# Kernel tuning notes

Measured on AMD Instinct MI355X. Metric: run time of the kernel, lower is better.

## Reference

```python
import jax, jax.numpy as jnp
import numpy as np

N = 8192
D = 512

def _row_normalize(m):
    # row-normalize; rows summing to 0 get inverse 0 (inf -> 0 in original)
    rs = m.sum(axis=1, keepdims=True)
    inv = jnp.where(rs == 0, 0.0, 1.0 / rs)
    return m * inv

def setup_inputs() -> dict:
    key = jax.random.key(0)
    k1, k2 = jax.random.split(key)
    qf = jax.random.normal(k1, (N, D), dtype=jnp.float32)
    gf = jax.random.normal(k2, (N, D), dtype=jnp.float32)
    return {"qf": qf, "gf": gf}

def reference(qf, gf):
    # feature = row-normalized squared difference  [N, D]
    feature = _row_normalize((qf - gf) ** 2)
    # adj[i, j] = ||feature_i - feature_j||^2, via GEMM expansion
    sq = jnp.sum(feature * feature, axis=-1)                  # [N]
    adj = sq[:, None] + sq[None, :] - 2.0 * (feature @ feature.T)  # [N, N]
    # symmetrize: elementwise max(adj, adj.T) (equivalent to the masked mix)
    adj = jnp.maximum(adj, adj.T)
    # add identity and row-normalize
    adj = adj + jnp.eye(N, dtype=adj.dtype)
    adj = _row_normalize(adj)
    return adj, feature
```

## Files before the change

### kernel.cpp

```cpp
#include <hip/hip_runtime.h>
#include <hip/hip_bf16.h>

#define N 8192
#define D 512

typedef __attribute__((ext_vector_type(8))) short short8;
typedef __attribute__((ext_vector_type(4))) float f32x4;

__device__ __forceinline__ float block_reduce_256(float v, float* red) {
    #pragma unroll
    for (int o = 1; o < 64; o <<= 1) v += __shfl_xor(v, o, 64);
    int w = threadIdx.x >> 6;
    if ((threadIdx.x & 63) == 0) red[w] = v;
    __syncthreads();
    float tot = red[0] + red[1] + red[2] + red[3];
    __syncthreads();
    return tot;
}

__global__ void feature_kernel(const float* __restrict__ qf, const float* __restrict__ gf,
                               float* __restrict__ feat, __hip_bfloat16* __restrict__ featb,
                               float* __restrict__ sq) {
    __shared__ float red[4];
    int row = blockIdx.x, t = threadIdx.x;
    const float2* q2 = (const float2*)(qf + (size_t)row * D);
    const float2* g2 = (const float2*)(gf + (size_t)row * D);
    float2 qv = q2[t], gv = g2[t];
    float a = qv.x - gv.x, b = qv.y - gv.y;
    float va = a * a, vb = b * b;
    float rs = block_reduce_256(va + vb, red);
    float inv = (rs == 0.0f) ? 0.0f : 1.0f / rs;
    float fa = va * inv, fb = vb * inv;
    ((float2*)(feat + (size_t)row * D))[t] = make_float2(fa, fb);
    __hip_bfloat162 h;
    h.x = __float2bfloat16(fa);
    h.y = __float2bfloat16(fb);
    ((__hip_bfloat162*)(featb + (size_t)row * D))[t] = h;
    float tot = block_reduce_256(fa * fa + fb * fb, red);
    if (t == 0) sq[row] = tot;
}

__global__ void colsum_partial_kernel(const float* __restrict__ feat, float* __restrict__ partial) {
    int b = blockIdx.x, t = threadIdx.x;
    const float* fp = feat + (size_t)b * 128 * D;
    float a0 = 0.f, a1 = 0.f;
    for (int r = 0; r < 128; ++r) {
        a0 += fp[r * D + t];
        a1 += fp[r * D + t + 256];
    }
    partial[b * D + t] = a0;
    partial[b * D + t + 256] = a1;
}

__global__ void finalize_kernel(const float* __restrict__ partial, const float* __restrict__ sq,
                                float* __restrict__ cvec, float* __restrict__ Sval) {
    __shared__ float red[4];
    int t = threadIdx.x;
    if (blockIdx.x == 0) {
        float a0 = 0.f, a1 = 0.f;
        for (int b = 0; b < 64; ++b) {
            a0 += partial[b * D + t];
            a1 += partial[b * D + t + 256];
        }
        cvec[t] = a0;
        cvec[t + 256] = a1;
    } else {
        float s = 0.f;
        for (int k = 0; k < N / 256; ++k) s += sq[t + 256 * k];
        float tot = block_reduce_256(s, red);
        if (t == 0) Sval[0] = tot;
    }
}

__global__ void rowinv_kernel(const float* __restrict__ feat, const float* __restrict__ sq,
                              const float* __restrict__ cvec, const float* __restrict__ Sval,
                              float* __restrict__ rowinv) {
    __shared__ float red[4];
    int row = blockIdx.x, t = threadIdx.x;
    float2 f = ((const float2*)(feat + (size_t)row * D))[t];
    float2 c = ((const float2*)cvec)[t];
    float dot = block_reduce_256(f.x * c.x + f.y * c.y, red);
    if (t == 0) {
        float rs = (float)N * sq[row] + Sval[0] - 2.0f * dot + 1.0f;
        rowinv[row] = (rs == 0.0f) ? 0.0f : 1.0f / rs;
    }
}

__global__ __launch_bounds__(512, 2) void adj_gemm_kernel(const __hip_bfloat16* __restrict__ featb,
                                                          const float* __restrict__ sq,
                                                          const float* __restrict__ rowinv,
                                                          float* __restrict__ out) {
    __shared__ __align__(16) char lds[131072];
    int wg = blockIdx.x;
    int id = (wg & 7) * 128 + (wg >> 3);
    int bx = id & 31, by = id >> 5;
    int rowBase = by * 256, colBase = bx * 256;

    int t = threadIdx.x, lane = t & 63, w = t >> 6;
    int wr = w >> 2, wc = w & 3, g = lane >> 4;

    f32x4 acc[8][4];
    #pragma unroll
    for (int m = 0; m < 8; ++m)
        #pragma unroll
        for (int n = 0; n < 4; ++n) acc[m][n] = (f32x4){0.f, 0.f, 0.f, 0.f};

    int srow = t >> 3, scol = t & 7;
    const __hip_bfloat16* gA = featb + (size_t)(rowBase + srow) * D + scol * 8;
    const __hip_bfloat16* gB = featb + (size_t)(colBase + srow) * D + scol * 8;
    int wo0 = srow * 128 + ((scol ^ (srow & 7)) * 16);

    int arow = wr * 128 + (lane & 15);
    int brow = wc * 64 + (lane & 15);
    int swzc = lane & 7;

    short8 ra[4], rb[4];
    #pragma unroll
    for (int q = 0; q < 4; ++q) {
        ra[q] = *(const short8*)(gA + (size_t)q * 64 * D);
        rb[q] = *(const short8*)(gB + (size_t)q * 64 * D);
    }
    #pragma unroll
    for (int q = 0; q < 4; ++q) {
        *(short8*)(lds + wo0 + q * 8192) = ra[q];
        *(short8*)(lds + 65536 + wo0 + q * 8192) = rb[q];
    }
    __syncthreads();

    int cur = 0;
    for (int ks = 0; ks < 8; ++ks) {
        if (ks < 7) {
            int k0 = (ks + 1) * 64;
            #pragma unroll
            for (int q = 0; q < 4; ++q) {
                ra[q] = *(const short8*)(gA + (size_t)q * 64 * D + k0);
                rb[q] = *(const short8*)(gB + (size_t)q * 64 * D + k0);
            }
        }
        const char* pA = lds + cur * 32768;
        const char* pB = lds + 65536 + cur * 32768;
        #pragma unroll
        for (int kk = 0; kk < 2; ++kk) {
            int ca = ((kk * 4 + g) ^ swzc) * 16;
            short8 bf[4];
            #pragma unroll
            for (int n = 0; n < 4; ++n)
                bf[n] = *(const short8*)(pB + (brow + 16 * n) * 128 + ca);
            #pragma unroll
            for (int m = 0; m < 8; ++m) {
                short8 af = *(const short8*)(pA + (arow + 16 * m) * 128 + ca);
                #pragma unroll
                for (int n = 0; n < 4; ++n)
                    acc[m][n] = __builtin_amdgcn_mfma_f32_16x16x32_bf16(af, bf[n], acc[m][n], 0, 0, 0);
            }
        }
        if (ks < 7) {
            char* wA = lds + (cur ^ 1) * 32768;
            char* wB = lds + 65536 + (cur ^ 1) * 32768;
            #pragma unroll
            for (int q = 0; q < 4; ++q) {
                *(short8*)(wA + wo0 + q * 8192) = ra[q];
                *(short8*)(wB + wo0 + q * 8192) = rb[q];
            }
        }
        __syncthreads();
        cur ^= 1;
    }

    float sqj[4];
    int jcol[4];
    #pragma unroll
    for (int n = 0; n < 4; ++n) {
        jcol[n] = colBase + wc * 64 + n * 16 + (lane & 15);
        sqj[n] = sq[jcol[n]];
    }
    #pragma unroll
    for (int m = 0; m < 8; ++m) {
        int ibase = rowBase + wr * 128 + m * 16 + g * 4;
        #pragma unroll
        for (int rI = 0; rI < 4; ++rI) {
            int i = ibase + rI;
            float si = sq[i], ri = rowinv[i];
            size_t ro = (size_t)i * N;
            #pragma unroll
            for (int n = 0; n < 4; ++n) {
                float pre = si + sqj[n] - 2.0f * acc[m][n][rI] + (i == jcol[n] ? 1.0f : 0.0f);
                out[ro + jcol[n]] = pre * ri;
            }
        }
    }
}

extern "C" void kernel_launch(void* const* d_in, const int* in_sizes, int n_in,
                              void* d_out, int out_size, void* d_ws, size_t ws_size,
                              hipStream_t stream) {
    const float* qf = (const float*)d_in[0];
    const float* gf = (const float*)d_in[1];
    float* out = (float*)d_out;
    float* feat = out + (size_t)N * N;

    char* wsb = (char*)d_ws;
    __hip_bfloat16* featb = (__hip_bfloat16*)wsb;
    float* sq      = (float*)(wsb + 8388608);
    float* partial = (float*)(wsb + 8388608 + 32768);
    float* cvec    = (float*)(wsb + 8388608 + 32768 + 131072);
    float* Sval    = (float*)(wsb + 8388608 + 32768 + 131072 + 2048);
    float* rowinv  = (float*)(wsb + 8388608 + 32768 + 131072 + 2048 + 64);

    feature_kernel<<<N, 256, 0, stream>>>(qf, gf, feat, featb, sq);
    colsum_partial_kernel<<<64, 256, 0, stream>>>(feat, partial);
    finalize_kernel<<<2, 256, 0, stream>>>(partial, sq, cvec, Sval);
    rowinv_kernel<<<N, 256, 0, stream>>>(feat, sq, cvec, Sval, rowinv);
    adj_gemm_kernel<<<1024, 512, 0, stream>>>(featb, sq, rowinv, out);
}
```

Before: 135.0 us.

## Use direct global-to-LDS loads with triple-buffered K pipeline in adjacency GEMM

Replaces the register-staged double-buffered GEMM mainloop with global_load_lds direct-to-LDS copies into three buffers of K=32 slices, using explicit vmcnt waits and barriers so loads run ahead of compute. It also raises MFMA wave priority with setprio and changes launch bounds to one workgroup per CU with a smaller LDS footprint. The goal is to remove the VGPR round trip and the LDS store instructions and to keep more loads in flight. In exchange it adds a second barrier per iteration, uses a smaller K step, and gives up the two-workgroup occupancy hint.

```diff
diff --git a/kernel.cpp b/kernel.cpp
--- a/kernel.cpp
+++ b/kernel.cpp
@@ -86,11 +86,11 @@
     }
 }
 
-__global__ __launch_bounds__(512, 2) void adj_gemm_kernel(const __hip_bfloat16* __restrict__ featb,
+__global__ __launch_bounds__(512, 1) void adj_gemm_kernel(const __hip_bfloat16* __restrict__ featb,
                                                           const float* __restrict__ sq,
                                                           const float* __restrict__ rowinv,
                                                           float* __restrict__ out) {
-    __shared__ __align__(16) char lds[131072];
+    __shared__ __align__(16) char lds[98304];
     int wg = blockIdx.x;
     int id = (wg & 7) * 128 + (wg >> 3);
     int bx = id & 31, by = id >> 5;
@@ -105,67 +105,67 @@
         #pragma unroll
         for (int n = 0; n < 4; ++n) acc[m][n] = (f32x4){0.f, 0.f, 0.f, 0.f};
 
-    int srow = t >> 3, scol = t & 7;
-    const __hip_bfloat16* gA = featb + (size_t)(rowBase + srow) * D + scol * 8;
-    const __hip_bfloat16* gB = featb + (size_t)(colBase + srow) * D + scol * 8;
-    int wo0 = srow * 128 + ((scol ^ (srow & 7)) * 16);
-
-    int arow = wr * 128 + (lane & 15);
-    int brow = wc * 64 + (lane & 15);
-    int swzc = lane & 7;
-
-    short8 ra[4], rb[4];
-    #pragma unroll
-    for (int q = 0; q < 4; ++q) {
-        ra[q] = *(const short8*)(gA + (size_t)q * 64 * D);
-        rb[q] = *(const short8*)(gB + (size_t)q * 64 * D);
-    }
-    #pragma unroll
-    for (int q = 0; q < 4; ++q) {
-        *(short8*)(lds + wo0 + q * 8192) = ra[q];
-        *(short8*)(lds + 65536 + wo0 + q * 8192) = rb[q];
-    }
-    __syncthreads();
-
-    int cur = 0;
-    for (int ks = 0; ks < 8; ++ks) {
-        if (ks < 7) {
-            int k0 = (ks + 1) * 64;
-            #pragma unroll
-            for (int q = 0; q < 4; ++q) {
-                ra[q] = *(const short8*)(gA + (size_t)q * 64 * D + k0);
-                rb[q] = *(const short8*)(gB + (size_t)q * 64 * D + k0);
-            }
-        }
-        const char* pA = lds + cur * 32768;
-        const char* pB = lds + 65536 + cur * 32768;
-        #pragma unroll
-        for (int kk = 0; kk < 2; ++kk) {
-            int ca = ((kk * 4 + g) ^ swzc) * 16;
-            short8 bf[4];
+    int j0 = w * 2, j1 = w * 2 + 1;
+    int rA0 = j0 * 16 + (lane >> 2), rA1 = j1 * 16 + (lane >> 2);
+    int cc = lane & 3;
+    int cg0 = cc ^ (rA0 & 3), cg1 = cc ^ (rA1 & 3);
+    const __hip_bfloat16* gA0 = featb + (size_t)(rowBase + rA0) * D + cg0 * 8;
+    const __hip_bfloat16* gA1 = featb + (size_t)(rowBase + rA1) * D + cg1 * 8;
+    const __hip_bfloat16* gB0 = featb + (size_t)(colBase + rA0) * D + cg0 * 8;
+    const __hip_bfloat16* gB1 = featb + (size_t)(colBase + rA1) * D + cg1 * 8;
+    char* ldsA = lds;
+    char* ldsB = lds + 49152;
+    int dA0 = j0 * 1024, dA1 = j1 * 1024;
+
+#define STAGE(p, kb) do { \
+    __builtin_amdgcn_global_load_lds((const void*)(gA0 + (kb)), (void*)(ldsA + (p) * 16384 + dA0), 16, 0, 0); \
+    __builtin_amdgcn_global_load_lds((const void*)(gA1 + (kb)), (void*)(ldsA + (p) * 16384 + dA1), 16, 0, 0); \
+    __builtin_amdgcn_global_load_lds((const void*)(gB0 + (kb)), (void*)(ldsB + (p) * 16384 + dA0), 16, 0, 0); \
+    __builtin_amdgcn_global_load_lds((const void*)(gB1 + (kb)), (void*)(ldsB + (p) * 16384 + dA1), 16, 0, 0); \
+} while (0)
+
+    STAGE(0, 0);
+    STAGE(1, 32);
+    STAGE(2, 64);
+
+    int ca = ((g ^ (lane & 3)) << 4);
+    int arow0 = wr * 128 + (lane & 15);
+    int brow0 = wc * 64 + (lane & 15);
+
+    for (int kt = 0; kt < 16; ++kt) {
+        if (kt <= 13)      asm volatile("s_waitcnt vmcnt(8)" ::: "memory");
+        else if (kt == 14) asm volatile("s_waitcnt vmcnt(4)" ::: "memory");
+        else               asm volatile("s_waitcnt vmcnt(0)" ::: "memory");
+        __builtin_amdgcn_s_barrier();
+        __builtin_amdgcn_sched_barrier(0);
+
+        int p = kt % 3;
+        const char* pA = ldsA + p * 16384;
+        const char* pB = ldsB + p * 16384;
+        short8 bf[4], af[8];
+        #pragma unroll
+        for (int n = 0; n < 4; ++n)
+            bf[n] = *(const short8*)(pB + (brow0 + 16 * n) * 64 + ca);
+        #pragma unroll
+        for (int m = 0; m < 8; ++m)
+            af[m] = *(const short8*)(pA + (arow0 + 16 * m) * 64 + ca);
+
+        __builtin_amdgcn_s_setprio(1);
+        #pragma unroll
+        for (int m = 0; m < 8; ++m)
             #pragma unroll
             for (int n = 0; n < 4; ++n)
-                bf[n] = *(const short8*)(pB + (brow + 16 * n) * 128 + ca);
-            #pragma unroll
-            for (int m = 0; m < 8; ++m) {
-                short8 af = *(const short8*)(pA + (arow + 16 * m) * 128 + ca);
-                #pragma unroll
-                for (int n = 0; n < 4; ++n)
-                    acc[m][n] = __builtin_amdgcn_mfma_f32_16x16x32_bf16(af, bf[n], acc[m][n], 0, 0, 0);
-            }
-        }
-        if (ks < 7) {
-            char* wA = lds + (cur ^ 1) * 32768;
-            char* wB = lds + 65536 + (cur ^ 1) * 32768;
-            #pragma unroll
-            for (int q = 0; q < 4; ++q) {
-                *(short8*)(wA + wo0 + q * 8192) = ra[q];
-                *(short8*)(wB + wo0 + q * 8192) = rb[q];
-            }
-        }
-        __syncthreads();
-        cur ^= 1;
-    }
+                acc[m][n] = __builtin_amdgcn_mfma_f32_16x16x32_bf16(af[m], bf[n], acc[m][n], 0, 0, 0);
+        __builtin_amdgcn_s_setprio(0);
+
+        asm volatile("s_waitcnt lgkmcnt(0)" ::: "memory");
+        __builtin_amdgcn_sched_barrier(0);
+        __builtin_amdgcn_s_barrier();
+        __builtin_amdgcn_sched_barrier(0);
+
+        if (kt < 13) STAGE(p, (kt + 3) * 32);
+    }
+#undef STAGE
 
     float sqj[4];
     int jcol[4];
```

Result: slower. 142.4 us (+5.5%).
